# Optimization experiments

Measured on AMD Instinct MI355X. Metric: run time of the kernel, lower is better.

The kernel has to match this reference:

```python
import jax, jax.numpy as jnp
import numpy as np
import math

KH = KW = 3
STRIDE = 1
PAD = 1
DIL = 1
C_IN = 256
C_OUT = 256
RANK = 32
BATCH = 16
H = W = 56


def setup_inputs() -> dict:
    key = jax.random.key(0)
    kx, kg, kh_, kb = jax.random.split(key, 4)
    x = jax.random.normal(kx, (BATCH, C_IN, H, W), dtype=jnp.float32)
    k2 = KH * KW
    bg = 1.0 / math.sqrt(C_IN)
    bh = 1.0 / math.sqrt(RANK)
    G = jax.random.uniform(kg, (k2, RANK, C_IN), minval=-bg, maxval=bg, dtype=jnp.float32)
    Hm = jax.random.uniform(kh_, (k2, C_OUT, RANK), minval=-bh, maxval=bh, dtype=jnp.float32)
    bias = jax.random.uniform(kb, (C_OUT,), minval=-bg, maxval=bg, dtype=jnp.float32)
    return {"x": x, "G": G, "Hm": Hm, "bias": bias}


def reference(x, G, Hm, bias):
    # Low-rank conv: per kernel position k, project patch through G[k] (rank) then H[k] (out),
    # then MEAN over the k2 positions (matches the original's .mean(dim=0)).
    b, c, h, w = x.shape
    h_out = (h + 2 * PAD - DIL * (KH - 1) - 1) // STRIDE + 1
    w_out = (h + 2 * PAD - DIL * (KW - 1) - 1) // STRIDE + 1  # original uses h here; square input
    xp = jnp.pad(x, ((0, 0), (0, 0), (PAD, PAD), (PAD, PAD)))
    acc = jnp.zeros((b, Hm.shape[1], h_out, w_out), dtype=x.dtype)
    for i in range(KH):
        for j in range(KW):
            k = i * KW + j
            # strided patch view for kernel offset (i, j): [b, c, h_out, w_out]
            patch = xp[:, :,
                       i * DIL:i * DIL + (h_out - 1) * STRIDE + 1:STRIDE,
                       j * DIL:j * DIL + (w_out - 1) * STRIDE + 1:STRIDE]
            t = jnp.einsum('bchw,rc->brhw', patch, G[k])      # rank projection
            acc = acc + jnp.einsum('brhw,or->bohw', t, Hm[k])  # out projection
    out = acc / (KH * KW) + bias[None, :, None, None]
    return out
```

## Files before the change

### kernel.cpp

```cpp
#include <hip/hip_runtime.h>
#include <stdint.h>


#define BATCH 16
#define CIN   256
#define COUT  256
#define RANK  32
#define HH    56
#define WW    56
#define SP    (HH*WW)
#define YP    58
#define XP    58
#define PCELL (YP*XP)
#define PLANE (BATCH*PCELL)

typedef __bf16 bf16x8 __attribute__((ext_vector_type(8)));
typedef float  f32x4  __attribute__((ext_vector_type(4)));

#define OFF_T9 0
#define OFF_GB 31002624
#define OFF_HB (OFF_GB + 147456)

#define RING_U4 (9 * 16 * 228 * 4)
#define PREP_N  (147456 + RING_U4)

__device__ __forceinline__ uint16_t bfbits(float f) {
  __bf16 h = (__bf16)f;
  return __builtin_bit_cast(uint16_t, h);
}

__global__ __launch_bounds__(256) void k_prep(const float* __restrict__ G,
                                              const float* __restrict__ Hm,
                                              uint16_t* __restrict__ G_bf,
                                              uint16_t* __restrict__ Hm_bf,
                                              uint16_t* __restrict__ T9) {
  int i = blockIdx.x * 256 + threadIdx.x;
  if (i < 73728)  { G_bf[i] = bfbits(G[i]); return; }
  if (i < 147456) { Hm_bf[i - 73728] = bfbits(Hm[i - 73728]); return; }
  int j = i - 147456;
  if (j >= RING_U4) return;
  int v = j & 3, cell = j >> 2;
  int tb = cell / 228, c = cell % 228;
  int y, xx;
  if      (c < 58)  { y = 0;       xx = c;       }
  else if (c < 116) { y = 57;      xx = c - 58;  }
  else if (c < 172) { y = c - 115; xx = 0;       }
  else              { y = c - 171; xx = 57;      }
  uint16_t* base = T9 + ((size_t)tb * PCELL + y * XP + xx) * 32;
  uint4 z; z.x = z.y = z.z = z.w = 0u;
  ((uint4*)base)[v] = z;
}

__global__ __launch_bounds__(384, 3) void k_fused1(const float* __restrict__ x,
                                                   const uint16_t* __restrict__ G_bf,
                                                   uint16_t* __restrict__ T9) {
  __shared__ uint16_t xs[32 * 264];
  const int tid = threadIdx.x;
  const int wave = tid >> 6, lane = tid & 63;
  const int q = lane >> 4, t = lane & 15;

  bf16x8 A[3][8];
  {
    const uint16_t* gb = G_bf + (size_t)(wave * 48 + t) * CIN + q * 8;
#pragma unroll
    for (int i = 0; i < 3; ++i)
#pragma unroll
      for (int ks = 0; ks < 8; ++ks)
        A[i][ks] = *(const bf16x8*)(gb + (size_t)i * 16 * CIN + ks * 32);
  }

#pragma unroll 1
  for (int item = blockIdx.x; item < 1568; item += 512) {
    const int b = item / 98, ch = item - b * 98;

#pragma unroll 1
    for (int u = tid; u < 1024; u += 384) {
      const int s = u & 31, cg = u >> 5;
      const float* xr = x + ((size_t)(b * CIN + cg * 8)) * SP + ch * 32 + s;
      bf16x8 v;
#pragma unroll
      for (int e = 0; e < 8; ++e)
        ((__bf16*)&v)[e] = (__bf16)xr[(size_t)e * SP];
      *(bf16x8*)&xs[s * 264 + cg * 8] = v;
    }
    __syncthreads();

#pragma unroll 1
    for (int nt = 0; nt < 2; ++nt) {
      bf16x8 Bf[8];
#pragma unroll
      for (int ks = 0; ks < 8; ++ks)
        Bf[ks] = *(const bf16x8*)&xs[(nt * 16 + t) * 264 + ks * 32 + q * 8];

      f32x4 acc[3];
#pragma unroll
      for (int i = 0; i < 3; ++i) acc[i] = (f32x4){0.f, 0.f, 0.f, 0.f};
#pragma unroll
      for (int ks = 0; ks < 8; ++ks)
#pragma unroll
        for (int i = 0; i < 3; ++i)
          acc[i] = __builtin_amdgcn_mfma_f32_16x16x32_bf16(A[i][ks], Bf[ks], acc[i], 0, 0, 0);

      const int p = ch * 32 + nt * 16 + t;
      const int h = p / WW, w = p - (p / WW) * WW;
      const size_t cellbase = ((size_t)b * PCELL + (h + 1) * XP + (w + 1)) * 32;
#pragma unroll
      for (int i = 0; i < 3; ++i) {
        const int kr0 = wave * 48 + i * 16 + q * 4;
        const int tap = kr0 >> 5, r = kr0 & 31;
        uint2 pv;
        pv.x = (uint32_t)bfbits(acc[i][0]) | ((uint32_t)bfbits(acc[i][1]) << 16);
        pv.y = (uint32_t)bfbits(acc[i][2]) | ((uint32_t)bfbits(acc[i][3]) << 16);
        *(uint2*)(T9 + (size_t)tap * PLANE * 32 + cellbase + r) = pv;
      }
    }
    __syncthreads();
  }
}

__global__ __launch_bounds__(512, 4) void k_stage2(const uint16_t* __restrict__ T9,
                                                   const uint16_t* __restrict__ Hm_bf,
                                                   const float* __restrict__ bias,
                                                   float* __restrict__ out) {
  const int wave = threadIdx.x >> 6, lane = threadIdx.x & 63;
  const int q = lane >> 4, t = lane & 15;

  bf16x8 Bf[9][2];
  float bv[2];
#pragma unroll
  for (int j = 0; j < 2; ++j) {
    const int o = wave * 32 + j * 16 + t;
    bv[j] = bias[o];
#pragma unroll
    for (int tap = 0; tap < 9; ++tap)
      Bf[tap][j] = *(const bf16x8*)(Hm_bf + ((size_t)(tap * COUT + o)) * RANK + q * 8);
  }

#pragma unroll 1
  for (int mt = blockIdx.x; mt < 3136; mt += 512) {
    const int p0 = mt * 16;
    const int b = p0 / SP, s0 = p0 - b * SP;
    const int sa = s0 + t;
    const int ha = sa / WW, wa = sa - ha * WW;
    const uint16_t* abase = T9 + ((size_t)(b * PCELL + ha * XP + wa)) * 32 + q * 8;

    f32x4 acc[2];
    acc[0] = (f32x4){0.f, 0.f, 0.f, 0.f};
    acc[1] = (f32x4){0.f, 0.f, 0.f, 0.f};
#pragma unroll
    for (int tap = 0; tap < 9; ++tap) {
      const int di = tap / 3, dj = tap % 3;
      bf16x8 af = *(const bf16x8*)(abase + (size_t)tap * PLANE * 32 + (di * XP + dj) * 32);
      acc[0] = __builtin_amdgcn_mfma_f32_16x16x32_bf16(af, Bf[0 + tap][0], acc[0], 0, 0, 0);
      acc[1] = __builtin_amdgcn_mfma_f32_16x16x32_bf16(af, Bf[0 + tap][1], acc[1], 0, 0, 0);
    }

    const int sd = s0 + q * 4;
#pragma unroll
    for (int j = 0; j < 2; ++j) {
      const int o = wave * 32 + j * 16 + t;
      f32x4 v = acc[j] * (1.0f / 9.0f) + bv[j];
      *(f32x4*)(out + ((size_t)(b * COUT + o)) * SP + sd) = v;
    }
  }
}

extern "C" void kernel_launch(void* const* d_in, const int* in_sizes, int n_in,
                              void* d_out, int out_size, void* d_ws, size_t ws_size,
                              hipStream_t stream) {
  const float* x    = (const float*)d_in[0];
  const float* G    = (const float*)d_in[1];
  const float* Hm   = (const float*)d_in[2];
  const float* bias = (const float*)d_in[3];
  float* out = (float*)d_out;
  char* ws = (char*)d_ws;

  uint16_t* T9    = (uint16_t*)(ws + OFF_T9);
  uint16_t* G_bf  = (uint16_t*)(ws + OFF_GB);
  uint16_t* Hm_bf = (uint16_t*)(ws + OFF_HB);

  k_prep<<<PREP_N / 256, 256, 0, stream>>>(G, Hm, G_bf, Hm_bf, T9);
  k_fused1<<<512, 384, 0, stream>>>(x, G_bf, T9);
  k_stage2<<<512, 512, 0, stream>>>(T9, Hm_bf, bias, out);
}
```

Measured before the change: 141.6 us.

## Use one tile per block, vectorize x loads, and remap stage2 tiles per XCD

k_fused1 now launches 784 blocks, each handling a single 64-pixel tile. This replaces the grid-stride loop over 32-pixel tiles, and x is read with float4 vector loads before conversion to bf16. k_stage2 processes two 16-pixel subtiles per iteration, issuing four MFMAs per tap, and assigns a contiguous range of tiles to each XCD. This improves L2 locality for the overlapping tap reads. The changes aim to cut per-tile loop and sync overhead and to raise load efficiency, at the cost of more LDS and registers per block.

```diff
diff --git a/kernel.cpp b/kernel.cpp
--- a/kernel.cpp
+++ b/kernel.cpp
@@ -54,11 +54,14 @@
 __global__ __launch_bounds__(384, 3) void k_fused1(const float* __restrict__ x,
                                                    const uint16_t* __restrict__ G_bf,
                                                    uint16_t* __restrict__ T9) {
-  __shared__ uint16_t xs[32 * 264];
+  __shared__ uint16_t xs[64 * 264];
   const int tid = threadIdx.x;
   const int wave = tid >> 6, lane = tid & 63;
   const int q = lane >> 4, t = lane & 15;
 
+  const int b  = blockIdx.x / 49;
+  const int ch = blockIdx.x - b * 49;
+
   bf16x8 A[3][8];
   {
     const uint16_t* gb = G_bf + (size_t)(wave * 48 + t) * CIN + q * 8;
@@ -70,51 +73,52 @@
   }
 
 #pragma unroll 1
-  for (int item = blockIdx.x; item < 1568; item += 512) {
-    const int b = item / 98, ch = item - b * 98;
+  for (int u = tid; u < 512; u += 384) {
+    const int s4 = u & 15, cg = u >> 4;
+    const float* xr = x + ((size_t)(b * CIN + cg * 8)) * SP + ch * 64 + s4 * 4;
+    f32x4 f[8];
+#pragma unroll
+    for (int e = 0; e < 8; ++e)
+      f[e] = *(const f32x4*)(xr + (size_t)e * SP);
+#pragma unroll
+    for (int p = 0; p < 4; ++p) {
+      bf16x8 v;
+#pragma unroll
+      for (int e = 0; e < 8; ++e)
+        ((__bf16*)&v)[e] = (__bf16)f[e][p];
+      *(bf16x8*)&xs[(s4 * 4 + p) * 264 + cg * 8] = v;
+    }
+  }
+  __syncthreads();
 
 #pragma unroll 1
-    for (int u = tid; u < 1024; u += 384) {
-      const int s = u & 31, cg = u >> 5;
-      const float* xr = x + ((size_t)(b * CIN + cg * 8)) * SP + ch * 32 + s;
-      bf16x8 v;
-#pragma unroll
-      for (int e = 0; e < 8; ++e)
-        ((__bf16*)&v)[e] = (__bf16)xr[(size_t)e * SP];
-      *(bf16x8*)&xs[s * 264 + cg * 8] = v;
-    }
-    __syncthreads();
-
-#pragma unroll 1
-    for (int nt = 0; nt < 2; ++nt) {
-      bf16x8 Bf[8];
-#pragma unroll
-      for (int ks = 0; ks < 8; ++ks)
-        Bf[ks] = *(const bf16x8*)&xs[(nt * 16 + t) * 264 + ks * 32 + q * 8];
-
-      f32x4 acc[3];
-#pragma unroll
-      for (int i = 0; i < 3; ++i) acc[i] = (f32x4){0.f, 0.f, 0.f, 0.f};
-#pragma unroll
-      for (int ks = 0; ks < 8; ++ks)
-#pragma unroll
-        for (int i = 0; i < 3; ++i)
-          acc[i] = __builtin_amdgcn_mfma_f32_16x16x32_bf16(A[i][ks], Bf[ks], acc[i], 0, 0, 0);
-
-      const int p = ch * 32 + nt * 16 + t;
-      const int h = p / WW, w = p - (p / WW) * WW;
-      const size_t cellbase = ((size_t)b * PCELL + (h + 1) * XP + (w + 1)) * 32;
-#pragma unroll
-      for (int i = 0; i < 3; ++i) {
-        const int kr0 = wave * 48 + i * 16 + q * 4;
-        const int tap = kr0 >> 5, r = kr0 & 31;
-        uint2 pv;
-        pv.x = (uint32_t)bfbits(acc[i][0]) | ((uint32_t)bfbits(acc[i][1]) << 16);
-        pv.y = (uint32_t)bfbits(acc[i][2]) | ((uint32_t)bfbits(acc[i][3]) << 16);
-        *(uint2*)(T9 + (size_t)tap * PLANE * 32 + cellbase + r) = pv;
-      }
-    }
-    __syncthreads();
+  for (int nt = 0; nt < 4; ++nt) {
+    bf16x8 Bf[8];
+#pragma unroll
+    for (int ks = 0; ks < 8; ++ks)
+      Bf[ks] = *(const bf16x8*)&xs[(nt * 16 + t) * 264 + ks * 32 + q * 8];
+
+    f32x4 acc[3];
+#pragma unroll
+    for (int i = 0; i < 3; ++i) acc[i] = (f32x4){0.f, 0.f, 0.f, 0.f};
+#pragma unroll
+    for (int ks = 0; ks < 8; ++ks)
+#pragma unroll
+      for (int i = 0; i < 3; ++i)
+        acc[i] = __builtin_amdgcn_mfma_f32_16x16x32_bf16(A[i][ks], Bf[ks], acc[i], 0, 0, 0);
+
+    const int p = ch * 64 + nt * 16 + t;
+    const int h = p / WW, w = p - (p / WW) * WW;
+    const size_t cellbase = ((size_t)b * PCELL + (h + 1) * XP + (w + 1)) * 32;
+#pragma unroll
+    for (int i = 0; i < 3; ++i) {
+      const int kr0 = wave * 48 + i * 16 + q * 4;
+      const int tap = kr0 >> 5, r = kr0 & 31;
+      uint2 pv;
+      pv.x = (uint32_t)bfbits(acc[i][0]) | ((uint32_t)bfbits(acc[i][1]) << 16);
+      pv.y = (uint32_t)bfbits(acc[i][2]) | ((uint32_t)bfbits(acc[i][3]) << 16);
+      *(uint2*)(T9 + (size_t)tap * PLANE * 32 + cellbase + r) = pv;
+    }
   }
 }
 
@@ -125,6 +129,10 @@
   const int wave = threadIdx.x >> 6, lane = threadIdx.x & 63;
   const int q = lane >> 4, t = lane & 15;
 
+  const int bid = (int)blockIdx.x;
+  const int xcd = bid & 7, pr = bid >> 3;
+  const int mt2base = xcd * 196 + pr * 2;
+
   bf16x8 Bf[9][2];
   float bv[2];
 #pragma unroll
@@ -137,30 +145,48 @@
   }
 
 #pragma unroll 1
-  for (int mt = blockIdx.x; mt < 3136; mt += 512) {
-    const int p0 = mt * 16;
+  for (int it = 0; it < 2; ++it) {
+    const int mt2 = mt2base + it;
+    const int p0 = mt2 * 32;
     const int b = p0 / SP, s0 = p0 - b * SP;
-    const int sa = s0 + t;
-    const int ha = sa / WW, wa = sa - ha * WW;
-    const uint16_t* abase = T9 + ((size_t)(b * PCELL + ha * XP + wa)) * 32 + q * 8;
-
-    f32x4 acc[2];
-    acc[0] = (f32x4){0.f, 0.f, 0.f, 0.f};
-    acc[1] = (f32x4){0.f, 0.f, 0.f, 0.f};
+
+    const uint16_t* abase0;
+    const uint16_t* abase1;
+    {
+      const int sa0 = s0 + t;
+      const int ha0 = sa0 / WW, wa0 = sa0 - ha0 * WW;
+      abase0 = T9 + ((size_t)(b * PCELL + ha0 * XP + wa0)) * 32 + q * 8;
+      const int sa1 = s0 + 16 + t;
+      const int ha1 = sa1 / WW, wa1 = sa1 - ha1 * WW;
+      abase1 = T9 + ((size_t)(b * PCELL + ha1 * XP + wa1)) * 32 + q * 8;
+    }
+
+    f32x4 acc00 = (f32x4){0.f, 0.f, 0.f, 0.f};
+    f32x4 acc01 = (f32x4){0.f, 0.f, 0.f, 0.f};
+    f32x4 acc10 = (f32x4){0.f, 0.f, 0.f, 0.f};
+    f32x4 acc11 = (f32x4){0.f, 0.f, 0.f, 0.f};
 #pragma unroll
     for (int tap = 0; tap < 9; ++tap) {
       const int di = tap / 3, dj = tap % 3;
-      bf16x8 af = *(const bf16x8*)(abase + (size_t)tap * PLANE * 32 + (di * XP + dj) * 32);
-      acc[0] = __builtin_amdgcn_mfma_f32_16x16x32_bf16(af, Bf[0 + tap][0], acc[0], 0, 0, 0);
-      acc[1] = __builtin_amdgcn_mfma_f32_16x16x32_bf16(af, Bf[0 + tap][1], acc[1], 0, 0, 0);
-    }
-
-    const int sd = s0 + q * 4;
+      const size_t toff = (size_t)tap * PLANE * 32 + (di * XP + dj) * 32;
+      bf16x8 a0 = *(const bf16x8*)(abase0 + toff);
+      bf16x8 a1 = *(const bf16x8*)(abase1 + toff);
+      acc00 = __builtin_amdgcn_mfma_f32_16x16x32_bf16(a0, Bf[tap][0], acc00, 0, 0, 0);
+      acc01 = __builtin_amdgcn_mfma_f32_16x16x32_bf16(a0, Bf[tap][1], acc01, 0, 0, 0);
+      acc10 = __builtin_amdgcn_mfma_f32_16x16x32_bf16(a1, Bf[tap][0], acc10, 0, 0, 0);
+      acc11 = __builtin_amdgcn_mfma_f32_16x16x32_bf16(a1, Bf[tap][1], acc11, 0, 0, 0);
+    }
+
+    const int sd0 = s0 + q * 4;
+    const int sd1 = s0 + 16 + q * 4;
 #pragma unroll
     for (int j = 0; j < 2; ++j) {
       const int o = wave * 32 + j * 16 + t;
-      f32x4 v = acc[j] * (1.0f / 9.0f) + bv[j];
-      *(f32x4*)(out + ((size_t)(b * COUT + o)) * SP + sd) = v;
+      float* orow = out + ((size_t)(b * COUT + o)) * SP;
+      f32x4 v0 = (j == 0 ? acc00 : acc01) * (1.0f / 9.0f) + bv[j];
+      f32x4 v1 = (j == 0 ? acc10 : acc11) * (1.0f / 9.0f) + bv[j];
+      *(f32x4*)(orow + sd0) = v0;
+      *(f32x4*)(orow + sd1) = v1;
     }
   }
 }
@@ -180,6 +206,6 @@
   uint16_t* Hm_bf = (uint16_t*)(ws + OFF_HB);
 
   k_prep<<<PREP_N / 256, 256, 0, stream>>>(G, Hm, G_bf, Hm_bf, T9);
-  k_fused1<<<512, 384, 0, stream>>>(x, G_bf, T9);
-  k_stage2<<<512, 512, 0, stream>>>(T9, Hm_bf, bias, out);
-}
+  k_fused1<<<784, 384, 0, stream>>>(x, G_bf, T9);
+  k_stage2<<<784, 512, 0, stream>>>(T9, Hm_bf, bias, out);
+}
```

Measured after the change: 152.1 us. 7.4% more time.
